# Kernel tuning notes

Measured on AMD Instinct MI355X. Metric: run time of the kernel, lower is better.

The kernel has to match this reference:

```python
import jax, jax.numpy as jnp
import numpy as np

DIM = 1024
NUM_EXPERTS = 8
N_TOKENS = 8192


def setup_inputs() -> dict:
    key = jax.random.key(0)
    ks = jax.random.split(key, 6)
    z_real = jax.random.normal(ks[0], (N_TOKENS, DIM), dtype=jnp.float32)
    z_imag = jax.random.normal(ks[1], (N_TOKENS, DIM), dtype=jnp.float32)
    # gate: nn.Linear(2*dim, E) -> weight [E, 2*dim], bias [E]
    Wg = jax.random.normal(ks[2], (NUM_EXPERTS, 2 * DIM), dtype=jnp.float32) * (1.0 / np.sqrt(2 * DIM))
    bg = jnp.zeros((NUM_EXPERTS,), dtype=jnp.float32)
    # experts: per-expert real/imag square weights [E, dim, dim] (nn.Linear layout: [out, in])
    Wr = jax.random.normal(ks[3], (NUM_EXPERTS, DIM, DIM), dtype=jnp.float32) * (1.0 / np.sqrt(DIM))
    Wi = jax.random.normal(ks[4], (NUM_EXPERTS, DIM, DIM), dtype=jnp.float32) * (1.0 / np.sqrt(DIM))
    return {"z_real": z_real, "z_imag": z_imag, "Wg": Wg, "bg": bg, "Wr": Wr, "Wi": Wi}


def reference(z_real, z_imag, Wg, bg, Wr, Wi):
    # gate over concat(real, imag)
    z_flat = jnp.concatenate([z_real, z_imag], axis=-1)            # [N, 2D]
    gates = jax.nn.softmax(z_flat @ Wg.T + bg, axis=-1)            # [N, E]
    # all-expert complex linear: y = x @ W^T with W [E, out, in]
    rr = jnp.einsum('ni,eoi->neo', z_real, Wr)                     # real @ Wr
    ii = jnp.einsum('ni,eoi->neo', z_imag, Wi)                     # imag @ Wi
    ri = jnp.einsum('ni,eoi->neo', z_imag, Wr)                     # imag @ Wr
    ir = jnp.einsum('ni,eoi->neo', z_real, Wi)                     # real @ Wi
    out_r = jnp.einsum('ne,neo->no', gates, rr - ii)               # [N, D]
    out_i = jnp.einsum('ne,neo->no', gates, ri + ir)               # [N, D]
    return jnp.stack([out_r, out_i], axis=0)                       # [2, N, D]
```

## Files before the change

kernel.cpp:

```cpp
#include <hip/hip_runtime.h>
#include <hip/hip_bf16.h>

#define NTOK 8192
#define DIM 1024
#define NEXP 8
#define NT 256
#define BK 64

typedef float f32x4 __attribute__((ext_vector_type(4)));
typedef short s16x8 __attribute__((ext_vector_type(8)));
typedef unsigned short u16;
typedef unsigned short u16x4 __attribute__((ext_vector_type(4)));

__device__ __forceinline__ u16 f2bf(float f) {
    __hip_bfloat16 h = __float2bfloat16(f);
    return *reinterpret_cast<u16*>(&h);
}
__device__ __forceinline__ float bf2f(u16 u) {
    unsigned v = ((unsigned)u) << 16;
    return __uint_as_float(v);
}

#define GLOAD16(gsrc, ldst)                                                     \
    __builtin_amdgcn_global_load_lds(                                           \
        (const __attribute__((address_space(1))) void*)(gsrc),                  \
        (__attribute__((address_space(3))) void*)(ldst), 16, 0, 0)

#define MFMA16(a, b, c) __builtin_amdgcn_mfma_f32_16x16x32_bf16((a), (b), (c), 0, 0, 0)
#define SGB() __builtin_amdgcn_sched_barrier(0)

__global__ __launch_bounds__(256) void gates_kernel(
    const float* __restrict__ zr, const float* __restrict__ zi,
    const float* __restrict__ Wg, const float* __restrict__ bg,
    float* __restrict__ gates)
{
    const int wave = threadIdx.x >> 6, lane = threadIdx.x & 63;
    const int n = blockIdx.x * 4 + wave;

    float v[32];
    const float* zrp = zr + (size_t)n * DIM;
    const float* zip = zi + (size_t)n * DIM;
#pragma unroll
    for (int j = 0; j < 16; ++j) v[j] = zrp[j * 64 + lane];
#pragma unroll
    for (int j = 0; j < 16; ++j) v[16 + j] = zip[j * 64 + lane];

    float s[NEXP];
#pragma unroll
    for (int e = 0; e < NEXP; ++e) {
        const float* wrow = Wg + (size_t)e * (2 * DIM);
        float a = 0.f;
#pragma unroll
        for (int j = 0; j < 32; ++j) a += v[j] * wrow[j * 64 + lane];
#pragma unroll
        for (int m = 32; m; m >>= 1) a += __shfl_xor(a, m);
        s[e] = a + bg[e];
    }
    float mx = s[0];
#pragma unroll
    for (int e = 1; e < NEXP; ++e) mx = fmaxf(mx, s[e]);
    float p[NEXP], sum = 0.f;
#pragma unroll
    for (int e = 0; e < NEXP; ++e) { p[e] = expf(s[e] - mx); sum += p[e]; }
    const float inv = 1.f / sum;
    if (lane == 0) {
#pragma unroll
        for (int e = 0; e < NEXP; ++e) gates[(size_t)n * NEXP + e] = p[e] * inv;
    }
}

__global__ __launch_bounds__(256) void cvt4_kernel(
    const float* __restrict__ zr, const float* __restrict__ zi,
    const float* __restrict__ Wr, const float* __restrict__ Wi,
    u16* __restrict__ zr16, u16* __restrict__ zi16,
    u16* __restrict__ Wr16, u16* __restrict__ Wi16)
{
    const size_t total = (size_t)NEXP * DIM * DIM / 4;
    for (size_t i = (size_t)blockIdx.x * 256 + threadIdx.x; i < total;
         i += (size_t)gridDim.x * 256) {
        f32x4 a = ((const f32x4*)zr)[i];
        f32x4 b = ((const f32x4*)zi)[i];
        f32x4 c = ((const f32x4*)Wr)[i];
        f32x4 d = ((const f32x4*)Wi)[i];
        u16x4 pa, pb, pc, pd;
#pragma unroll
        for (int j = 0; j < 4; ++j) {
            pa[j] = f2bf(a[j]); pb[j] = f2bf(b[j]);
            pc[j] = f2bf(c[j]); pd[j] = f2bf(d[j]);
        }
        ((u16x4*)zr16)[i] = pa;
        ((u16x4*)zi16)[i] = pb;
        ((u16x4*)Wr16)[i] = pc;
        ((u16x4*)Wi16)[i] = pd;
    }
}

__global__ __launch_bounds__(512, 2) void moe_gemm8(
    const u16* __restrict__ zr16, const u16* __restrict__ zi16,
    const u16* __restrict__ Wr16, const u16* __restrict__ Wi16,
    const float* __restrict__ gates, float* __restrict__ out)
{
    extern __shared__ u16 lds[];

    const int linear = blockIdx.x + 32 * (blockIdx.y + 4 * blockIdx.z);
    const int xcd = linear & 7;
    const int bm = xcd * 4 + ((linear >> 3) & 3);
    const int grp2 = linear >> 5;
    const int bn = grp2 & 3;
    const int sel = grp2 >> 2;

    const int tid = threadIdx.x;
    const int lane = tid & 63;
    const int wid = tid >> 6;
    const int wr = wid >> 2;
    const int wc = wid & 3;

    const int srow = tid >> 3;
    const int schunk = (tid & 7) ^ (srow & 7);
    int arow[4], gidx[4], brow[4];
#pragma unroll
    for (int j = 0; j < 4; ++j) {
        const int gr = bm * 256 + srow + j * 64;
        arow[j] = gr * DIM + schunk * 8;
        gidx[j] = gr * NEXP;
        brow[j] = (bn * 256 + srow + j * 64) * DIM + schunk * 8;
    }

    const int cg = lane >> 4;
    const int l7 = lane & 7;
    const int ach0 = (cg ^ l7) * 8;
    const int ach1 = ((4 + cg) ^ l7) * 8;
    const int arbase = (wr * 128 + (lane & 15)) * BK;
    const int brbase = (wc * 64 + (lane & 15)) * BK;

    f32x4 acc[8][4];
#pragma unroll
    for (int m = 0; m < 8; ++m)
#pragma unroll
        for (int n = 0; n < 4; ++n) acc[m][n] = (f32x4){0.f, 0.f, 0.f, 0.f};

    const u16* Asrc = sel ? zi16 : zr16;
    const u16* Bseg = Wr16;
    float sg[4];
#pragma unroll
    for (int j = 0; j < 4; ++j) sg[j] = gates[gidx[j]];

    {
        s16x8 ga[4];
#pragma unroll
        for (int j = 0; j < 4; ++j) ga[j] = *(const s16x8*)(Asrc + arow[j]);
#pragma unroll
        for (int i = 0; i < 4; ++i)
            GLOAD16(Bseg + brow[i], &lds[32768 + (i * 512 + tid) * 8]);
#pragma unroll
        for (int i = 0; i < 4; ++i)
            GLOAD16(Bseg + brow[i] + 64, &lds[32768 + 16384 + (i * 512 + tid) * 8]);
#pragma unroll
        for (int j = 0; j < 4; ++j) {
            s16x8 w;
#pragma unroll
            for (int q = 0; q < 8; ++q)
                w[q] = (short)f2bf(bf2f((u16)ga[j][q]) * sg[j]);
            *(s16x8*)&lds[(tid + j * 512) * 8] = w;
        }
        asm volatile("s_waitcnt vmcnt(4) lgkmcnt(0)" ::: "memory");
        __builtin_amdgcn_s_barrier();
    }

    int br = 0;
#pragma unroll 1
    for (int t = 0; t < NT; ++t) {
        const int tn1 = t + 1, tn2 = t + 2;
        if ((tn1 & 15) == 0) {
            const int seg = tn1 >> 4;
            const int e = (seg >> 1) & 7;
            const int half = seg & 1;
            Asrc = (half ^ sel) ? zi16 : zr16;
            const float sgn = (sel == 0 && half == 1) ? -1.f : 1.f;
#pragma unroll
            for (int j = 0; j < 4; ++j) sg[j] = sgn * gates[gidx[j] + e];
        }
        if ((tn2 & 15) == 0) {
            const int seg = tn2 >> 4;
            const int e = (seg >> 1) & 7;
            Bseg = ((seg & 1) ? Wi16 : Wr16) + (size_t)e * DIM * DIM;
        }
        const int ka = (tn1 & 15) << 6;
        const int kb = (tn2 & 15) << 6;
        const int bs = (br + 2) % 3;
        const int ab = ((t & 1) << 14) + arbase;
        const int bb = 32768 + br * 16384 + brbase;
        const int sa = ((tn1 & 1) << 14);
        const int sbB = 32768 + bs * 16384;

        s16x8 ga[4];
#pragma unroll
        for (int j = 0; j < 4; ++j) ga[j] = *(const s16x8*)(Asrc + arow[j] + ka);
        GLOAD16(Bseg + brow[0] + kb, &lds[sbB + (0 * 512 + tid) * 8]);
        GLOAD16(Bseg + brow[1] + kb, &lds[sbB + (1 * 512 + tid) * 8]);
        GLOAD16(Bseg + brow[2] + kb, &lds[sbB + (2 * 512 + tid) * 8]);
        GLOAD16(Bseg + brow[3] + kb, &lds[sbB + (3 * 512 + tid) * 8]);

        s16x8 b0[4], a0[4], a1[4], b1[4], a2[4], a3[4];
#pragma unroll
        for (int n = 0; n < 4; ++n) b0[n] = *(const s16x8*)&lds[bb + n * 1024 + ach0];
#pragma unroll
        for (int m = 0; m < 4; ++m) a0[m] = *(const s16x8*)&lds[ab + m * 1024 + ach0];
#pragma unroll
        for (int m = 0; m < 4; ++m) a1[m] = *(const s16x8*)&lds[ab + (m + 4) * 1024 + ach0];
        SGB();
        __builtin_amdgcn_s_setprio(1);
#pragma unroll
        for (int m = 0; m < 4; ++m)
#pragma unroll
            for (int n = 0; n < 4; ++n) acc[m][n] = MFMA16(a0[m], b0[n], acc[m][n]);
        __builtin_amdgcn_s_setprio(0);

#pragma unroll
        for (int n = 0; n < 4; ++n) b1[n] = *(const s16x8*)&lds[bb + n * 1024 + ach1];
#pragma unroll
        for (int m = 0; m < 4; ++m) a2[m] = *(const s16x8*)&lds[ab + m * 1024 + ach1];
        SGB();
        __builtin_amdgcn_s_setprio(1);
#pragma unroll
        for (int m = 0; m < 4; ++m)
#pragma unroll
            for (int n = 0; n < 4; ++n) acc[m + 4][n] = MFMA16(a1[m], b0[n], acc[m + 4][n]);
        __builtin_amdgcn_s_setprio(0);

#pragma unroll
        for (int j = 0; j < 2; ++j) {
            s16x8 w;
#pragma unroll
            for (int q = 0; q < 8; ++q)
                w[q] = (short)f2bf(bf2f((u16)ga[j][q]) * sg[j]);
            *(s16x8*)&lds[sa + (tid + j * 512) * 8] = w;
        }
#pragma unroll
        for (int m = 0; m < 4; ++m) a3[m] = *(const s16x8*)&lds[ab + (m + 4) * 1024 + ach1];
        SGB();
        __builtin_amdgcn_s_setprio(1);
#pragma unroll
        for (int m = 0; m < 4; ++m)
#pragma unroll
            for (int n = 0; n < 4; ++n) acc[m][n] = MFMA16(a2[m], b1[n], acc[m][n]);
        __builtin_amdgcn_s_setprio(0);

#pragma unroll
        for (int j = 2; j < 4; ++j) {
            s16x8 w;
#pragma unroll
            for (int q = 0; q < 8; ++q)
                w[q] = (short)f2bf(bf2f((u16)ga[j][q]) * sg[j]);
            *(s16x8*)&lds[sa + (tid + j * 512) * 8] = w;
        }
        __builtin_amdgcn_s_setprio(1);
#pragma unroll
        for (int m = 0; m < 4; ++m)
#pragma unroll
            for (int n = 0; n < 4; ++n) acc[m + 4][n] = MFMA16(a3[m], b1[n], acc[m + 4][n]);
        __builtin_amdgcn_s_setprio(0);

        asm volatile("s_waitcnt vmcnt(4) lgkmcnt(0)" ::: "memory");
        __builtin_amdgcn_s_barrier();

        br = (br == 2) ? 0 : br + 1;
    }
    asm volatile("s_waitcnt vmcnt(0)" ::: "memory");

    float* op = out + (size_t)sel * NTOK * DIM;
    const int col0 = bn * 256 + wc * 64 + (lane & 15);
    const int row0 = bm * 256 + wr * 128 + ((lane >> 4) << 2);
#pragma unroll
    for (int m = 0; m < 8; ++m)
#pragma unroll
        for (int n = 0; n < 4; ++n)
#pragma unroll
            for (int j = 0; j < 4; ++j)
                op[(size_t)(row0 + m * 16 + j) * DIM + col0 + n * 16] = acc[m][n][j];
}

extern "C" void kernel_launch(void* const* d_in, const int* in_sizes, int n_in,
                              void* d_out, int out_size, void* d_ws, size_t ws_size,
                              hipStream_t stream) {
    const float* zr = (const float*)d_in[0];
    const float* zi = (const float*)d_in[1];
    const float* Wg = (const float*)d_in[2];
    const float* bg = (const float*)d_in[3];
    const float* Wr = (const float*)d_in[4];
    const float* Wi = (const float*)d_in[5];
    float* out = (float*)d_out;

    const size_t NELEM = (size_t)NEXP * DIM * DIM;
    u16* zr16 = (u16*)d_ws;
    u16* zi16 = zr16 + NELEM;
    u16* Wr16 = zi16 + NELEM;
    u16* Wi16 = Wr16 + NELEM;
    float* gates = (float*)(Wi16 + NELEM);

    cvt4_kernel<<<2048, 256, 0, stream>>>(zr, zi, Wr, Wi, zr16, zi16, Wr16, Wi16);
    gates_kernel<<<NTOK / 4, 256, 0, stream>>>(zr, zi, Wg, bg, gates);

    hipFuncSetAttribute((const void*)moe_gemm8,
                        hipFuncAttributeMaxDynamicSharedMemorySize, 163840);
    dim3 grid(NTOK / 256, DIM / 256, 2);
    moe_gemm8<<<grid, 512, 163840, stream>>>(zr16, zi16, Wr16, Wi16, gates, out);
}
```

Before: 542.6 us.

## Restructure GEMM pipeline: triple-buffer A, double-buffer B, prefetch first A fragments

Changes the shared-memory buffering in the MoE GEMM main loop. The scaled activation tile A is now triple-buffered and written two steps ahead, and the weight tile B is double-buffered and loaded one step ahead. The first A register fragments for the next iteration are loaded before the loop-end barrier, and the barrier waits on all global loads while leaving some LDS reads outstanding. The goal is to hide LDS read latency across the barrier and to spread the activation scaling work between MFMA groups. The trade-offs are a shorter global-load lookahead for B and extra registers held for the prefetched fragments.

```diff
diff --git a/kernel.cpp b/kernel.cpp
--- a/kernel.cpp
+++ b/kernel.cpp
@@ -95,7 +95,7 @@
     }
 }
 
-__global__ __launch_bounds__(512, 2) void moe_gemm8(
+__global__ __launch_bounds__(512, 2) void moe_gemm12(
     const u16* __restrict__ zr16, const u16* __restrict__ zi16,
     const u16* __restrict__ Wr16, const u16* __restrict__ Wi16,
     const float* __restrict__ gates, float* __restrict__ out)
@@ -146,33 +146,43 @@
     for (int j = 0; j < 4; ++j) sg[j] = gates[gidx[j]];
 
     {
-        s16x8 ga[4];
-#pragma unroll
-        for (int j = 0; j < 4; ++j) ga[j] = *(const s16x8*)(Asrc + arow[j]);
-#pragma unroll
-        for (int i = 0; i < 4; ++i)
-            GLOAD16(Bseg + brow[i], &lds[32768 + (i * 512 + tid) * 8]);
-#pragma unroll
-        for (int i = 0; i < 4; ++i)
-            GLOAD16(Bseg + brow[i] + 64, &lds[32768 + 16384 + (i * 512 + tid) * 8]);
+        s16x8 ga0[4], ga1[4];
 #pragma unroll
         for (int j = 0; j < 4; ++j) {
-            s16x8 w;
-#pragma unroll
-            for (int q = 0; q < 8; ++q)
-                w[q] = (short)f2bf(bf2f((u16)ga[j][q]) * sg[j]);
-            *(s16x8*)&lds[(tid + j * 512) * 8] = w;
-        }
-        asm volatile("s_waitcnt vmcnt(4) lgkmcnt(0)" ::: "memory");
+            ga0[j] = *(const s16x8*)(Asrc + arow[j]);
+            ga1[j] = *(const s16x8*)(Asrc + arow[j] + BK);
+        }
+#pragma unroll
+        for (int q = 0; q < 4; ++q)
+            GLOAD16(Bseg + brow[q], &lds[49152 + (q * 512 + tid) * 8]);
+#pragma unroll
+        for (int j = 0; j < 4; ++j) {
+            s16x8 w0, w1;
+#pragma unroll
+            for (int e = 0; e < 8; ++e) {
+                w0[e] = (short)f2bf(bf2f((u16)ga0[j][e]) * sg[j]);
+                w1[e] = (short)f2bf(bf2f((u16)ga1[j][e]) * sg[j]);
+            }
+            *(s16x8*)&lds[(tid + j * 512) * 8] = w0;
+            *(s16x8*)&lds[16384 + (tid + j * 512) * 8] = w1;
+        }
+        asm volatile("s_waitcnt vmcnt(0) lgkmcnt(0)" ::: "memory");
         __builtin_amdgcn_s_barrier();
     }
 
-    int br = 0;
+    s16x8 a0p[4];
+#pragma unroll
+    for (int m = 0; m < 4; ++m)
+        a0p[m] = *(const s16x8*)&lds[arbase + m * 1024 + ach0];
+
+    int ars = 0;
+    int aws = 2;
+    int brs = 0;
 #pragma unroll 1
     for (int t = 0; t < NT; ++t) {
-        const int tn1 = t + 1, tn2 = t + 2;
-        if ((tn1 & 15) == 0) {
-            const int seg = tn1 >> 4;
+        const int t1 = t + 1, t2 = t + 2;
+        if ((t2 & 15) == 0) {
+            const int seg = t2 >> 4;
             const int e = (seg >> 1) & 7;
             const int half = seg & 1;
             Asrc = (half ^ sel) ? zi16 : zr16;
@@ -180,19 +190,21 @@
 #pragma unroll
             for (int j = 0; j < 4; ++j) sg[j] = sgn * gates[gidx[j] + e];
         }
-        if ((tn2 & 15) == 0) {
-            const int seg = tn2 >> 4;
+        if ((t1 & 15) == 0) {
+            const int seg = t1 >> 4;
             const int e = (seg >> 1) & 7;
             Bseg = ((seg & 1) ? Wi16 : Wr16) + (size_t)e * DIM * DIM;
         }
-        const int ka = (tn1 & 15) << 6;
-        const int kb = (tn2 & 15) << 6;
-        const int bs = (br + 2) % 3;
-        const int ab = ((t & 1) << 14) + arbase;
-        const int bb = 32768 + br * 16384 + brbase;
-        const int sa = ((tn1 & 1) << 14);
-        const int sbB = 32768 + bs * 16384;
-
+        const int ka = (t2 & 15) << 6;
+        const int kb = (t1 & 15) << 6;
+        const int ab = ars * 16384 + arbase;
+        const int bb = 49152 + brs * 16384 + brbase;
+        const int sa = aws * 16384;
+        const int sbB = 49152 + (brs ^ 1) * 16384;
+
+        s16x8 b0[4];
+#pragma unroll
+        for (int n = 0; n < 4; ++n) b0[n] = *(const s16x8*)&lds[bb + n * 1024 + ach0];
         s16x8 ga[4];
 #pragma unroll
         for (int j = 0; j < 4; ++j) ga[j] = *(const s16x8*)(Asrc + arow[j] + ka);
@@ -200,12 +212,7 @@
         GLOAD16(Bseg + brow[1] + kb, &lds[sbB + (1 * 512 + tid) * 8]);
         GLOAD16(Bseg + brow[2] + kb, &lds[sbB + (2 * 512 + tid) * 8]);
         GLOAD16(Bseg + brow[3] + kb, &lds[sbB + (3 * 512 + tid) * 8]);
-
-        s16x8 b0[4], a0[4], a1[4], b1[4], a2[4], a3[4];
-#pragma unroll
-        for (int n = 0; n < 4; ++n) b0[n] = *(const s16x8*)&lds[bb + n * 1024 + ach0];
-#pragma unroll
-        for (int m = 0; m < 4; ++m) a0[m] = *(const s16x8*)&lds[ab + m * 1024 + ach0];
+        s16x8 a1[4];
 #pragma unroll
         for (int m = 0; m < 4; ++m) a1[m] = *(const s16x8*)&lds[ab + (m + 4) * 1024 + ach0];
         SGB();
@@ -213,9 +220,18 @@
 #pragma unroll
         for (int m = 0; m < 4; ++m)
 #pragma unroll
-            for (int n = 0; n < 4; ++n) acc[m][n] = MFMA16(a0[m], b0[n], acc[m][n]);
+            for (int n = 0; n < 4; ++n) acc[m][n] = MFMA16(a0p[m], b0[n], acc[m][n]);
         __builtin_amdgcn_s_setprio(0);
 
+#pragma unroll
+        for (int j = 0; j < 2; ++j) {
+            s16x8 w;
+#pragma unroll
+            for (int e = 0; e < 8; ++e)
+                w[e] = (short)f2bf(bf2f((u16)ga[j][e]) * sg[j]);
+            *(s16x8*)&lds[sa + (tid + j * 512) * 8] = w;
+        }
+        s16x8 b1[4], a2[4];
 #pragma unroll
         for (int n = 0; n < 4; ++n) b1[n] = *(const s16x8*)&lds[bb + n * 1024 + ach1];
 #pragma unroll
@@ -229,13 +245,14 @@
         __builtin_amdgcn_s_setprio(0);
 
 #pragma unroll
-        for (int j = 0; j < 2; ++j) {
+        for (int j = 2; j < 4; ++j) {
             s16x8 w;
 #pragma unroll
-            for (int q = 0; q < 8; ++q)
-                w[q] = (short)f2bf(bf2f((u16)ga[j][q]) * sg[j]);
+            for (int e = 0; e < 8; ++e)
+                w[e] = (short)f2bf(bf2f((u16)ga[j][e]) * sg[j]);
             *(s16x8*)&lds[sa + (tid + j * 512) * 8] = w;
         }
+        s16x8 a3[4];
 #pragma unroll
         for (int m = 0; m < 4; ++m) a3[m] = *(const s16x8*)&lds[ab + (m + 4) * 1024 + ach1];
         SGB();
@@ -246,14 +263,11 @@
             for (int n = 0; n < 4; ++n) acc[m][n] = MFMA16(a2[m], b1[n], acc[m][n]);
         __builtin_amdgcn_s_setprio(0);
 
-#pragma unroll
-        for (int j = 2; j < 4; ++j) {
-            s16x8 w;
-#pragma unroll
-            for (int q = 0; q < 8; ++q)
-                w[q] = (short)f2bf(bf2f((u16)ga[j][q]) * sg[j]);
-            *(s16x8*)&lds[sa + (tid + j * 512) * 8] = w;
-        }
+        const int arn = (ars == 2) ? 0 : ars + 1;
+        const int abn = arn * 16384 + arbase;
+#pragma unroll
+        for (int m = 0; m < 4; ++m) a0p[m] = *(const s16x8*)&lds[abn + m * 1024 + ach0];
+        SGB();
         __builtin_amdgcn_s_setprio(1);
 #pragma unroll
         for (int m = 0; m < 4; ++m)
@@ -261,12 +275,14 @@
             for (int n = 0; n < 4; ++n) acc[m + 4][n] = MFMA16(a3[m], b1[n], acc[m + 4][n]);
         __builtin_amdgcn_s_setprio(0);
 
-        asm volatile("s_waitcnt vmcnt(4) lgkmcnt(0)" ::: "memory");
+        asm volatile("s_waitcnt vmcnt(0) lgkmcnt(4)" ::: "memory");
         __builtin_amdgcn_s_barrier();
 
-        br = (br == 2) ? 0 : br + 1;
-    }
-    asm volatile("s_waitcnt vmcnt(0)" ::: "memory");
+        ars = arn;
+        aws = (aws == 2) ? 0 : aws + 1;
+        brs ^= 1;
+    }
+    asm volatile("s_waitcnt vmcnt(0) lgkmcnt(0)" ::: "memory");
 
     float* op = out + (size_t)sel * NTOK * DIM;
     const int col0 = bn * 256 + wc * 64 + (lane & 15);
@@ -301,8 +317,8 @@
     cvt4_kernel<<<2048, 256, 0, stream>>>(zr, zi, Wr, Wi, zr16, zi16, Wr16, Wi16);
     gates_kernel<<<NTOK / 4, 256, 0, stream>>>(zr, zi, Wg, bg, gates);
 
-    hipFuncSetAttribute((const void*)moe_gemm8,
+    hipFuncSetAttribute((const void*)moe_gemm12,
                         hipFuncAttributeMaxDynamicSharedMemorySize, 163840);
     dim3 grid(NTOK / 256, DIM / 256, 2);
-    moe_gemm8<<<grid, 512, 163840, stream>>>(zr16, zi16, Wr16, Wi16, gates, out);
-}
+    moe_gemm12<<<grid, 512, 163840, stream>>>(zr16, zi16, Wr16, Wi16, gates, out);
+}
```

New measurement: 550.8 us. No clear change (+1.5%).

## Replace triple-buffered B pipeline with double-buffered ping-pong and extra barriers

Applied to the files above, without the earlier changes.

The B-operand prefetch moves from a three-deep ring (two tiles ahead) to a two-buffer ping-pong (one tile ahead), which cuts LDS use from 160 KB to 128 KB. The main loop is regrouped into two 8x4 MFMA phases, each with a partial lgkmcnt wait and a mid-phase workgroup barrier, in a ping-pong style schedule. The goal is tighter wave synchronisation and less LDS footprint. In exchange, global-load latency is hidden less deeply, a full vmcnt(0) wait now runs every iteration, and there are more barriers per tile.

```diff
diff --git a/kernel.cpp b/kernel.cpp
--- a/kernel.cpp
+++ b/kernel.cpp
@@ -95,7 +95,7 @@
     }
 }
 
-__global__ __launch_bounds__(512, 2) void moe_gemm8(
+__global__ __launch_bounds__(512, 2) void moe_gemm13(
     const u16* __restrict__ zr16, const u16* __restrict__ zi16,
     const u16* __restrict__ Wr16, const u16* __restrict__ Wi16,
     const float* __restrict__ gates, float* __restrict__ out)
@@ -146,127 +146,101 @@
     for (int j = 0; j < 4; ++j) sg[j] = gates[gidx[j]];
 
     {
-        s16x8 ga[4];
-#pragma unroll
-        for (int j = 0; j < 4; ++j) ga[j] = *(const s16x8*)(Asrc + arow[j]);
-#pragma unroll
-        for (int i = 0; i < 4; ++i)
-            GLOAD16(Bseg + brow[i], &lds[32768 + (i * 512 + tid) * 8]);
-#pragma unroll
-        for (int i = 0; i < 4; ++i)
-            GLOAD16(Bseg + brow[i] + 64, &lds[32768 + 16384 + (i * 512 + tid) * 8]);
+        s16x8 ga0[4];
+#pragma unroll
+        for (int j = 0; j < 4; ++j) ga0[j] = *(const s16x8*)(Asrc + arow[j]);
+#pragma unroll
+        for (int q = 0; q < 4; ++q)
+            GLOAD16(Bseg + brow[q], &lds[32768 + (q * 512 + tid) * 8]);
 #pragma unroll
         for (int j = 0; j < 4; ++j) {
             s16x8 w;
 #pragma unroll
-            for (int q = 0; q < 8; ++q)
-                w[q] = (short)f2bf(bf2f((u16)ga[j][q]) * sg[j]);
+            for (int e = 0; e < 8; ++e)
+                w[e] = (short)f2bf(bf2f((u16)ga0[j][e]) * sg[j]);
             *(s16x8*)&lds[(tid + j * 512) * 8] = w;
         }
-        asm volatile("s_waitcnt vmcnt(4) lgkmcnt(0)" ::: "memory");
-        __builtin_amdgcn_s_barrier();
-    }
-
-    int br = 0;
+        asm volatile("s_waitcnt vmcnt(0) lgkmcnt(0)" ::: "memory");
+        __builtin_amdgcn_s_barrier();
+    }
+
+    int buf = 0;
 #pragma unroll 1
     for (int t = 0; t < NT; ++t) {
-        const int tn1 = t + 1, tn2 = t + 2;
-        if ((tn1 & 15) == 0) {
-            const int seg = tn1 >> 4;
+        const int t1 = t + 1;
+        if ((t1 & 15) == 0) {
+            const int seg = t1 >> 4;
             const int e = (seg >> 1) & 7;
             const int half = seg & 1;
             Asrc = (half ^ sel) ? zi16 : zr16;
+            Bseg = (half ? Wi16 : Wr16) + (size_t)e * DIM * DIM;
             const float sgn = (sel == 0 && half == 1) ? -1.f : 1.f;
 #pragma unroll
             for (int j = 0; j < 4; ++j) sg[j] = sgn * gates[gidx[j] + e];
         }
-        if ((tn2 & 15) == 0) {
-            const int seg = tn2 >> 4;
-            const int e = (seg >> 1) & 7;
-            Bseg = ((seg & 1) ? Wi16 : Wr16) + (size_t)e * DIM * DIM;
-        }
-        const int ka = (tn1 & 15) << 6;
-        const int kb = (tn2 & 15) << 6;
-        const int bs = (br + 2) % 3;
-        const int ab = ((t & 1) << 14) + arbase;
-        const int bb = 32768 + br * 16384 + brbase;
-        const int sa = ((tn1 & 1) << 14);
-        const int sbB = 32768 + bs * 16384;
+        const int ka = (t1 & 15) << 6;
+        const int ab = buf * 16384 + arbase;
+        const int bb = 32768 + buf * 16384 + brbase;
+        const int sa = (buf ^ 1) * 16384;
+        const int sb = 32768 + (buf ^ 1) * 16384;
 
         s16x8 ga[4];
 #pragma unroll
         for (int j = 0; j < 4; ++j) ga[j] = *(const s16x8*)(Asrc + arow[j] + ka);
-        GLOAD16(Bseg + brow[0] + kb, &lds[sbB + (0 * 512 + tid) * 8]);
-        GLOAD16(Bseg + brow[1] + kb, &lds[sbB + (1 * 512 + tid) * 8]);
-        GLOAD16(Bseg + brow[2] + kb, &lds[sbB + (2 * 512 + tid) * 8]);
-        GLOAD16(Bseg + brow[3] + kb, &lds[sbB + (3 * 512 + tid) * 8]);
-
-        s16x8 b0[4], a0[4], a1[4], b1[4], a2[4], a3[4];
+        GLOAD16(Bseg + brow[0] + ka, &lds[sb + (0 * 512 + tid) * 8]);
+        GLOAD16(Bseg + brow[1] + ka, &lds[sb + (1 * 512 + tid) * 8]);
+        GLOAD16(Bseg + brow[2] + ka, &lds[sb + (2 * 512 + tid) * 8]);
+        GLOAD16(Bseg + brow[3] + ka, &lds[sb + (3 * 512 + tid) * 8]);
+
+        s16x8 b0[4], a01[8];
 #pragma unroll
         for (int n = 0; n < 4; ++n) b0[n] = *(const s16x8*)&lds[bb + n * 1024 + ach0];
 #pragma unroll
-        for (int m = 0; m < 4; ++m) a0[m] = *(const s16x8*)&lds[ab + m * 1024 + ach0];
-#pragma unroll
-        for (int m = 0; m < 4; ++m) a1[m] = *(const s16x8*)&lds[ab + (m + 4) * 1024 + ach0];
+        for (int m = 0; m < 8; ++m) a01[m] = *(const s16x8*)&lds[ab + m * 1024 + ach0];
+        asm volatile("s_waitcnt lgkmcnt(8)" ::: "memory");
+        SGB();
+        __builtin_amdgcn_s_barrier();
+        asm volatile("s_waitcnt lgkmcnt(0)" ::: "memory");
         SGB();
         __builtin_amdgcn_s_setprio(1);
 #pragma unroll
-        for (int m = 0; m < 4; ++m)
-#pragma unroll
-            for (int n = 0; n < 4; ++n) acc[m][n] = MFMA16(a0[m], b0[n], acc[m][n]);
+        for (int m = 0; m < 8; ++m)
+#pragma unroll
+            for (int n = 0; n < 4; ++n) acc[m][n] = MFMA16(a01[m], b0[n], acc[m][n]);
         __builtin_amdgcn_s_setprio(0);
-
+        SGB();
+        __builtin_amdgcn_s_barrier();
+
+        s16x8 b1[4], a23[8];
 #pragma unroll
         for (int n = 0; n < 4; ++n) b1[n] = *(const s16x8*)&lds[bb + n * 1024 + ach1];
 #pragma unroll
-        for (int m = 0; m < 4; ++m) a2[m] = *(const s16x8*)&lds[ab + m * 1024 + ach1];
+        for (int m = 0; m < 8; ++m) a23[m] = *(const s16x8*)&lds[ab + m * 1024 + ach1];
+#pragma unroll
+        for (int j = 0; j < 4; ++j) {
+            s16x8 w;
+#pragma unroll
+            for (int e = 0; e < 8; ++e)
+                w[e] = (short)f2bf(bf2f((u16)ga[j][e]) * sg[j]);
+            *(s16x8*)&lds[sa + (tid + j * 512) * 8] = w;
+        }
+        asm volatile("s_waitcnt lgkmcnt(8)" ::: "memory");
+        SGB();
+        __builtin_amdgcn_s_barrier();
+        asm volatile("s_waitcnt lgkmcnt(0)" ::: "memory");
         SGB();
         __builtin_amdgcn_s_setprio(1);
 #pragma unroll
-        for (int m = 0; m < 4; ++m)
-#pragma unroll
-            for (int n = 0; n < 4; ++n) acc[m + 4][n] = MFMA16(a1[m], b0[n], acc[m + 4][n]);
+        for (int m = 0; m < 8; ++m)
+#pragma unroll
+            for (int n = 0; n < 4; ++n) acc[m][n] = MFMA16(a23[m], b1[n], acc[m][n]);
         __builtin_amdgcn_s_setprio(0);
-
-#pragma unroll
-        for (int j = 0; j < 2; ++j) {
-            s16x8 w;
-#pragma unroll
-            for (int q = 0; q < 8; ++q)
-                w[q] = (short)f2bf(bf2f((u16)ga[j][q]) * sg[j]);
-            *(s16x8*)&lds[sa + (tid + j * 512) * 8] = w;
-        }
-#pragma unroll
-        for (int m = 0; m < 4; ++m) a3[m] = *(const s16x8*)&lds[ab + (m + 4) * 1024 + ach1];
-        SGB();
-        __builtin_amdgcn_s_setprio(1);
-#pragma unroll
-        for (int m = 0; m < 4; ++m)
-#pragma unroll
-            for (int n = 0; n < 4; ++n) acc[m][n] = MFMA16(a2[m], b1[n], acc[m][n]);
-        __builtin_amdgcn_s_setprio(0);
-
-#pragma unroll
-        for (int j = 2; j < 4; ++j) {
-            s16x8 w;
-#pragma unroll
-            for (int q = 0; q < 8; ++q)
-                w[q] = (short)f2bf(bf2f((u16)ga[j][q]) * sg[j]);
-            *(s16x8*)&lds[sa + (tid + j * 512) * 8] = w;
-        }
-        __builtin_amdgcn_s_setprio(1);
-#pragma unroll
-        for (int m = 0; m < 4; ++m)
-#pragma unroll
-            for (int n = 0; n < 4; ++n) acc[m + 4][n] = MFMA16(a3[m], b1[n], acc[m + 4][n]);
-        __builtin_amdgcn_s_setprio(0);
-
-        asm volatile("s_waitcnt vmcnt(4) lgkmcnt(0)" ::: "memory");
-        __builtin_amdgcn_s_barrier();
-
-        br = (br == 2) ? 0 : br + 1;
-    }
-    asm volatile("s_waitcnt vmcnt(0)" ::: "memory");
+        asm volatile("s_waitcnt vmcnt(0)" ::: "memory");
+        SGB();
+        __builtin_amdgcn_s_barrier();
+
+        buf ^= 1;
+    }
 
     float* op = out + (size_t)sel * NTOK * DIM;
     const int col0 = bn * 256 + wc * 64 + (lane & 15);
@@ -301,8 +275,8 @@
     cvt4_kernel<<<2048, 256, 0, stream>>>(zr, zi, Wr, Wi, zr16, zi16, Wr16, Wi16);
     gates_kernel<<<NTOK / 4, 256, 0, stream>>>(zr, zi, Wg, bg, gates);
 
-    hipFuncSetAttribute((const void*)moe_gemm8,
-                        hipFuncAttributeMaxDynamicSharedMemorySize, 163840);
+    hipFuncSetAttribute((const void*)moe_gemm13,
+                        hipFuncAttributeMaxDynamicSharedMemorySize, 131072);
     dim3 grid(NTOK / 256, DIM / 256, 2);
-    moe_gemm8<<<grid, 512, 163840, stream>>>(zr16, zi16, Wr16, Wi16, gates, out);
-}
+    moe_gemm13<<<grid, 512, 131072, stream>>>(zr16, zi16, Wr16, Wi16, gates, out);
+}
```

Measured after the change: 574.3 us. +5.8%, slower.

## Precompute gate-scaled bf16 activations per expert and stream both operands via LDS DMA

Applied to the files above, without the earlier changes.

Gates are now computed first, and a new prez kernel writes 16 gate-scaled bf16 copies of the activations (one per expert for real and imag), plus a negated Wi copy so the subtraction folds into the weights. The new GEMM loads A directly into LDS with global_load_lds (triple-buffered) instead of loading into registers, scaling, and storing, and uses finer-grained barriers between MFMA phases. This removes per-tile VALU scaling and register staging from the GEMM main loop. In exchange it writes and reads far more workspace (16x the activation volume, about 256MB in bf16) and adds a barrier-heavy schedule, and it falls back to the old path when the workspace is too small.

```diff
diff --git a/kernel.cpp b/kernel.cpp
--- a/kernel.cpp
+++ b/kernel.cpp
@@ -6,6 +6,7 @@
 #define NEXP 8
 #define NT 256
 #define BK 64
+#define NELEMZ ((size_t)NTOK * DIM)
 
 typedef float f32x4 __attribute__((ext_vector_type(4)));
 typedef short s16x8 __attribute__((ext_vector_type(8)));
@@ -69,13 +70,237 @@
     }
 }
 
+__global__ __launch_bounds__(256) void prez_kernel(
+    const float* __restrict__ zr, const float* __restrict__ zi,
+    const float* __restrict__ gates, u16* __restrict__ zvar)
+{
+    const size_t total = NELEMZ / 4;
+    for (size_t i = (size_t)blockIdx.x * 256 + threadIdx.x; i < total;
+         i += (size_t)gridDim.x * 256) {
+        const int n = (int)(i >> 8);
+        f32x4 a = ((const f32x4*)zr)[i];
+        f32x4 b = ((const f32x4*)zi)[i];
+        float g[NEXP];
+#pragma unroll
+        for (int e = 0; e < NEXP; ++e) g[e] = gates[(size_t)n * NEXP + e];
+#pragma unroll
+        for (int e = 0; e < NEXP; ++e) {
+            u16x4 pa, pb;
+#pragma unroll
+            for (int j = 0; j < 4; ++j) {
+                pa[j] = f2bf(a[j] * g[e]);
+                pb[j] = f2bf(b[j] * g[e]);
+            }
+            ((u16x4*)(zvar + (size_t)e * NELEMZ))[i] = pa;
+            ((u16x4*)(zvar + (size_t)(8 + e) * NELEMZ))[i] = pb;
+        }
+    }
+}
+
+__global__ __launch_bounds__(256) void wcvt3_kernel(
+    const float* __restrict__ Wr, const float* __restrict__ Wi,
+    u16* __restrict__ Wr16, u16* __restrict__ Wi16, u16* __restrict__ WiN16)
+{
+    const size_t total = NELEMZ / 4;
+    for (size_t i = (size_t)blockIdx.x * 256 + threadIdx.x; i < total;
+         i += (size_t)gridDim.x * 256) {
+        f32x4 c = ((const f32x4*)Wr)[i];
+        f32x4 d = ((const f32x4*)Wi)[i];
+        u16x4 pc, pd, pn;
+#pragma unroll
+        for (int j = 0; j < 4; ++j) {
+            pc[j] = f2bf(c[j]);
+            pd[j] = f2bf(d[j]);
+            pn[j] = f2bf(-d[j]);
+        }
+        ((u16x4*)Wr16)[i] = pc;
+        ((u16x4*)Wi16)[i] = pd;
+        ((u16x4*)WiN16)[i] = pn;
+    }
+}
+
+__global__ __launch_bounds__(512, 2) void moe_gemm14(
+    const u16* __restrict__ zvar,
+    const u16* __restrict__ Wr16, const u16* __restrict__ Wi16,
+    const u16* __restrict__ WiN16, float* __restrict__ out)
+{
+    extern __shared__ u16 lds[];
+
+    const int linear = blockIdx.x + 32 * (blockIdx.y + 4 * blockIdx.z);
+    const int xcd = linear & 7;
+    const int bm = xcd * 4 + ((linear >> 3) & 3);
+    const int grp2 = linear >> 5;
+    const int bn = grp2 & 3;
+    const int sel = grp2 >> 2;
+
+    const int tid = threadIdx.x;
+    const int lane = tid & 63;
+    const int wid = tid >> 6;
+    const int wr = wid >> 2;
+    const int wc = wid & 3;
+
+    const int srow = tid >> 3;
+    const int schunk = (tid & 7) ^ (srow & 7);
+    int arow[4], brow[4];
+#pragma unroll
+    for (int j = 0; j < 4; ++j) {
+        arow[j] = (bm * 256 + srow + j * 64) * DIM + schunk * 8;
+        brow[j] = (bn * 256 + srow + j * 64) * DIM + schunk * 8;
+    }
+
+    const int cg = lane >> 4;
+    const int l7 = lane & 7;
+    const int ach0 = (cg ^ l7) * 8;
+    const int ach1 = ((4 + cg) ^ l7) * 8;
+    const int arbase = (wr * 128 + (lane & 15)) * BK;
+    const int brbase = (wc * 64 + (lane & 15)) * BK;
+
+    f32x4 acc[8][4];
+#pragma unroll
+    for (int m = 0; m < 8; ++m)
+#pragma unroll
+        for (int n = 0; n < 4; ++n) acc[m][n] = (f32x4){0.f, 0.f, 0.f, 0.f};
+
+    const u16* Avar = zvar + (size_t)(sel ? 8 : 0) * NELEMZ;
+    const u16* Bh0 = Wr16;
+    const u16* Bh1 = sel ? Wi16 : WiN16;
+    const u16* Bseg = Bh0;
+
+    {
+#pragma unroll
+        for (int j = 0; j < 4; ++j) GLOAD16(Avar + arow[j], &lds[(j * 512 + tid) * 8]);
+#pragma unroll
+        for (int j = 0; j < 4; ++j) GLOAD16(Avar + arow[j] + BK, &lds[16384 + (j * 512 + tid) * 8]);
+#pragma unroll
+        for (int j = 0; j < 4; ++j) GLOAD16(Bseg + brow[j], &lds[49152 + (j * 512 + tid) * 8]);
+        asm volatile("s_waitcnt vmcnt(0)" ::: "memory");
+        __builtin_amdgcn_s_barrier();
+    }
+
+    int ars = 0;
+#pragma unroll 1
+    for (int t = 0; t < NT; ++t) {
+        const int t1 = t + 1, t2 = t + 2;
+        if ((t1 & 15) == 0) {
+            const int seg = t1 >> 4;
+            const int e = (seg >> 1) & 7;
+            Bseg = ((seg & 1) ? Bh1 : Bh0) + (size_t)e * DIM * DIM;
+        }
+        if ((t2 & 15) == 0) {
+            const int seg = t2 >> 4;
+            const int e = (seg >> 1) & 7;
+            const int half = seg & 1;
+            Avar = zvar + (size_t)(((half ^ sel) ? 8 : 0) + e) * NELEMZ;
+        }
+        const int kb1 = (t1 & 15) << 6;
+        const int ka2 = (t2 & 15) << 6;
+        const int aw = (ars == 0) ? 2 : ars - 1;
+        const int brs = t & 1;
+        const int ab = ars * 16384 + arbase;
+        const int bb = 49152 + brs * 16384 + brbase;
+        const int sa = aw * 16384;
+        const int sb = 49152 + (brs ^ 1) * 16384;
+
+        GLOAD16(Bseg + brow[0] + kb1, &lds[sb + (0 * 512 + tid) * 8]);
+        GLOAD16(Bseg + brow[1] + kb1, &lds[sb + (1 * 512 + tid) * 8]);
+        GLOAD16(Bseg + brow[2] + kb1, &lds[sb + (2 * 512 + tid) * 8]);
+        GLOAD16(Bseg + brow[3] + kb1, &lds[sb + (3 * 512 + tid) * 8]);
+        s16x8 b0[4], a0[4];
+#pragma unroll
+        for (int n = 0; n < 4; ++n) b0[n] = *(const s16x8*)&lds[bb + n * 1024 + ach0];
+#pragma unroll
+        for (int m = 0; m < 4; ++m) a0[m] = *(const s16x8*)&lds[ab + m * 1024 + ach0];
+        SGB();
+        __builtin_amdgcn_s_barrier();
+        asm volatile("s_waitcnt lgkmcnt(0)" ::: "memory");
+        SGB();
+        __builtin_amdgcn_s_setprio(1);
+#pragma unroll
+        for (int m = 0; m < 4; ++m)
+#pragma unroll
+            for (int n = 0; n < 4; ++n) acc[m][n] = MFMA16(a0[m], b0[n], acc[m][n]);
+        __builtin_amdgcn_s_setprio(0);
+        SGB();
+        __builtin_amdgcn_s_barrier();
+
+        GLOAD16(Avar + arow[0] + ka2, &lds[sa + (0 * 512 + tid) * 8]);
+        GLOAD16(Avar + arow[1] + ka2, &lds[sa + (1 * 512 + tid) * 8]);
+        GLOAD16(Avar + arow[2] + ka2, &lds[sa + (2 * 512 + tid) * 8]);
+        GLOAD16(Avar + arow[3] + ka2, &lds[sa + (3 * 512 + tid) * 8]);
+        s16x8 a1[4];
+#pragma unroll
+        for (int m = 0; m < 4; ++m) a1[m] = *(const s16x8*)&lds[ab + (m + 4) * 1024 + ach0];
+        SGB();
+        __builtin_amdgcn_s_barrier();
+        asm volatile("s_waitcnt lgkmcnt(0)" ::: "memory");
+        SGB();
+        __builtin_amdgcn_s_setprio(1);
+#pragma unroll
+        for (int m = 0; m < 4; ++m)
+#pragma unroll
+            for (int n = 0; n < 4; ++n) acc[m + 4][n] = MFMA16(a1[m], b0[n], acc[m + 4][n]);
+        __builtin_amdgcn_s_setprio(0);
+        SGB();
+        __builtin_amdgcn_s_barrier();
+
+        s16x8 b1[4], a2[4];
+#pragma unroll
+        for (int n = 0; n < 4; ++n) b1[n] = *(const s16x8*)&lds[bb + n * 1024 + ach1];
+#pragma unroll
+        for (int m = 0; m < 4; ++m) a2[m] = *(const s16x8*)&lds[ab + m * 1024 + ach1];
+        SGB();
+        __builtin_amdgcn_s_barrier();
+        asm volatile("s_waitcnt lgkmcnt(0)" ::: "memory");
+        SGB();
+        __builtin_amdgcn_s_setprio(1);
+#pragma unroll
+        for (int m = 0; m < 4; ++m)
+#pragma unroll
+            for (int n = 0; n < 4; ++n) acc[m][n] = MFMA16(a2[m], b1[n], acc[m][n]);
+        __builtin_amdgcn_s_setprio(0);
+        SGB();
+        __builtin_amdgcn_s_barrier();
+
+        s16x8 a3[4];
+#pragma unroll
+        for (int m = 0; m < 4; ++m) a3[m] = *(const s16x8*)&lds[ab + (m + 4) * 1024 + ach1];
+        SGB();
+        __builtin_amdgcn_s_barrier();
+        asm volatile("s_waitcnt lgkmcnt(0)" ::: "memory");
+        SGB();
+        __builtin_amdgcn_s_setprio(1);
+#pragma unroll
+        for (int m = 0; m < 4; ++m)
+#pragma unroll
+            for (int n = 0; n < 4; ++n) acc[m + 4][n] = MFMA16(a3[m], b1[n], acc[m + 4][n]);
+        __builtin_amdgcn_s_setprio(0);
+        asm volatile("s_waitcnt vmcnt(4)" ::: "memory");
+        SGB();
+        __builtin_amdgcn_s_barrier();
+
+        ars = (ars == 2) ? 0 : ars + 1;
+    }
+    asm volatile("s_waitcnt vmcnt(0)" ::: "memory");
+
+    float* op = out + (size_t)sel * NTOK * DIM;
+    const int col0 = bn * 256 + wc * 64 + (lane & 15);
+    const int row0 = bm * 256 + wr * 128 + ((lane >> 4) << 2);
+#pragma unroll
+    for (int m = 0; m < 8; ++m)
+#pragma unroll
+        for (int n = 0; n < 4; ++n)
+#pragma unroll
+            for (int j = 0; j < 4; ++j)
+                op[(size_t)(row0 + m * 16 + j) * DIM + col0 + n * 16] = acc[m][n][j];
+}
+
 __global__ __launch_bounds__(256) void cvt4_kernel(
     const float* __restrict__ zr, const float* __restrict__ zi,
     const float* __restrict__ Wr, const float* __restrict__ Wi,
     u16* __restrict__ zr16, u16* __restrict__ zi16,
     u16* __restrict__ Wr16, u16* __restrict__ Wi16)
 {
-    const size_t total = (size_t)NEXP * DIM * DIM / 4;
+    const size_t total = NELEMZ / 4;
     for (size_t i = (size_t)blockIdx.x * 256 + threadIdx.x; i < total;
          i += (size_t)gridDim.x * 256) {
         f32x4 a = ((const f32x4*)zr)[i];
@@ -101,20 +326,16 @@
     const float* __restrict__ gates, float* __restrict__ out)
 {
     extern __shared__ u16 lds[];
-
     const int linear = blockIdx.x + 32 * (blockIdx.y + 4 * blockIdx.z);
     const int xcd = linear & 7;
     const int bm = xcd * 4 + ((linear >> 3) & 3);
     const int grp2 = linear >> 5;
     const int bn = grp2 & 3;
     const int sel = grp2 >> 2;
-
     const int tid = threadIdx.x;
     const int lane = tid & 63;
     const int wid = tid >> 6;
-    const int wr = wid >> 2;
-    const int wc = wid & 3;
-
+    const int wr = wid >> 2, wc = wid & 3;
     const int srow = tid >> 3;
     const int schunk = (tid & 7) ^ (srow & 7);
     int arow[4], gidx[4], brow[4];
@@ -125,48 +346,39 @@
         gidx[j] = gr * NEXP;
         brow[j] = (bn * 256 + srow + j * 64) * DIM + schunk * 8;
     }
-
-    const int cg = lane >> 4;
-    const int l7 = lane & 7;
+    const int cg = lane >> 4, l7 = lane & 7;
     const int ach0 = (cg ^ l7) * 8;
     const int ach1 = ((4 + cg) ^ l7) * 8;
     const int arbase = (wr * 128 + (lane & 15)) * BK;
     const int brbase = (wc * 64 + (lane & 15)) * BK;
-
     f32x4 acc[8][4];
 #pragma unroll
     for (int m = 0; m < 8; ++m)
 #pragma unroll
         for (int n = 0; n < 4; ++n) acc[m][n] = (f32x4){0.f, 0.f, 0.f, 0.f};
-
     const u16* Asrc = sel ? zi16 : zr16;
     const u16* Bseg = Wr16;
     float sg[4];
 #pragma unroll
     for (int j = 0; j < 4; ++j) sg[j] = gates[gidx[j]];
-
     {
         s16x8 ga[4];
 #pragma unroll
         for (int j = 0; j < 4; ++j) ga[j] = *(const s16x8*)(Asrc + arow[j]);
 #pragma unroll
-        for (int i = 0; i < 4; ++i)
-            GLOAD16(Bseg + brow[i], &lds[32768 + (i * 512 + tid) * 8]);
-#pragma unroll
-        for (int i = 0; i < 4; ++i)
-            GLOAD16(Bseg + brow[i] + 64, &lds[32768 + 16384 + (i * 512 + tid) * 8]);
+        for (int i = 0; i < 4; ++i) GLOAD16(Bseg + brow[i], &lds[32768 + (i * 512 + tid) * 8]);
+#pragma unroll
+        for (int i = 0; i < 4; ++i) GLOAD16(Bseg + brow[i] + 64, &lds[32768 + 16384 + (i * 512 + tid) * 8]);
 #pragma unroll
         for (int j = 0; j < 4; ++j) {
             s16x8 w;
 #pragma unroll
-            for (int q = 0; q < 8; ++q)
-                w[q] = (short)f2bf(bf2f((u16)ga[j][q]) * sg[j]);
+            for (int q = 0; q < 8; ++q) w[q] = (short)f2bf(bf2f((u16)ga[j][q]) * sg[j]);
             *(s16x8*)&lds[(tid + j * 512) * 8] = w;
         }
         asm volatile("s_waitcnt vmcnt(4) lgkmcnt(0)" ::: "memory");
         __builtin_amdgcn_s_barrier();
     }
-
     int br = 0;
 #pragma unroll 1
     for (int t = 0; t < NT; ++t) {
@@ -187,12 +399,11 @@
         }
         const int ka = (tn1 & 15) << 6;
         const int kb = (tn2 & 15) << 6;
-        const int bs = (br + 2) % 3;
+        const int bs = (br == 0) ? 2 : br - 1;
         const int ab = ((t & 1) << 14) + arbase;
         const int bb = 32768 + br * 16384 + brbase;
         const int sa = ((tn1 & 1) << 14);
         const int sbB = 32768 + bs * 16384;
-
         s16x8 ga[4];
 #pragma unroll
         for (int j = 0; j < 4; ++j) ga[j] = *(const s16x8*)(Asrc + arow[j] + ka);
@@ -200,7 +411,6 @@
         GLOAD16(Bseg + brow[1] + kb, &lds[sbB + (1 * 512 + tid) * 8]);
         GLOAD16(Bseg + brow[2] + kb, &lds[sbB + (2 * 512 + tid) * 8]);
         GLOAD16(Bseg + brow[3] + kb, &lds[sbB + (3 * 512 + tid) * 8]);
-
         s16x8 b0[4], a0[4], a1[4], b1[4], a2[4], a3[4];
 #pragma unroll
         for (int n = 0; n < 4; ++n) b0[n] = *(const s16x8*)&lds[bb + n * 1024 + ach0];
@@ -215,7 +425,6 @@
 #pragma unroll
             for (int n = 0; n < 4; ++n) acc[m][n] = MFMA16(a0[m], b0[n], acc[m][n]);
         __builtin_amdgcn_s_setprio(0);
-
 #pragma unroll
         for (int n = 0; n < 4; ++n) b1[n] = *(const s16x8*)&lds[bb + n * 1024 + ach1];
 #pragma unroll
@@ -227,13 +436,11 @@
 #pragma unroll
             for (int n = 0; n < 4; ++n) acc[m + 4][n] = MFMA16(a1[m], b0[n], acc[m + 4][n]);
         __builtin_amdgcn_s_setprio(0);
-
 #pragma unroll
         for (int j = 0; j < 2; ++j) {
             s16x8 w;
 #pragma unroll
-            for (int q = 0; q < 8; ++q)
-                w[q] = (short)f2bf(bf2f((u16)ga[j][q]) * sg[j]);
+            for (int q = 0; q < 8; ++q) w[q] = (short)f2bf(bf2f((u16)ga[j][q]) * sg[j]);
             *(s16x8*)&lds[sa + (tid + j * 512) * 8] = w;
         }
 #pragma unroll
@@ -245,13 +452,11 @@
 #pragma unroll
             for (int n = 0; n < 4; ++n) acc[m][n] = MFMA16(a2[m], b1[n], acc[m][n]);
         __builtin_amdgcn_s_setprio(0);
-
 #pragma unroll
         for (int j = 2; j < 4; ++j) {
             s16x8 w;
 #pragma unroll
-            for (int q = 0; q < 8; ++q)
-                w[q] = (short)f2bf(bf2f((u16)ga[j][q]) * sg[j]);
+            for (int q = 0; q < 8; ++q) w[q] = (short)f2bf(bf2f((u16)ga[j][q]) * sg[j]);
             *(s16x8*)&lds[sa + (tid + j * 512) * 8] = w;
         }
         __builtin_amdgcn_s_setprio(1);
@@ -260,14 +465,11 @@
 #pragma unroll
             for (int n = 0; n < 4; ++n) acc[m + 4][n] = MFMA16(a3[m], b1[n], acc[m + 4][n]);
         __builtin_amdgcn_s_setprio(0);
-
         asm volatile("s_waitcnt vmcnt(4) lgkmcnt(0)" ::: "memory");
         __builtin_amdgcn_s_barrier();
-
         br = (br == 2) ? 0 : br + 1;
     }
     asm volatile("s_waitcnt vmcnt(0)" ::: "memory");
-
     float* op = out + (size_t)sel * NTOK * DIM;
     const int col0 = bn * 256 + wc * 64 + (lane & 15);
     const int row0 = bm * 256 + wr * 128 + ((lane >> 4) << 2);
@@ -291,18 +493,37 @@
     const float* Wi = (const float*)d_in[5];
     float* out = (float*)d_out;
 
-    const size_t NELEM = (size_t)NEXP * DIM * DIM;
-    u16* zr16 = (u16*)d_ws;
-    u16* zi16 = zr16 + NELEM;
-    u16* Wr16 = zi16 + NELEM;
-    u16* Wi16 = Wr16 + NELEM;
-    float* gates = (float*)(Wi16 + NELEM);
-
-    cvt4_kernel<<<2048, 256, 0, stream>>>(zr, zi, Wr, Wi, zr16, zi16, Wr16, Wi16);
-    gates_kernel<<<NTOK / 4, 256, 0, stream>>>(zr, zi, Wg, bg, gates);
-
-    hipFuncSetAttribute((const void*)moe_gemm8,
-                        hipFuncAttributeMaxDynamicSharedMemorySize, 163840);
-    dim3 grid(NTOK / 256, DIM / 256, 2);
-    moe_gemm8<<<grid, 512, 163840, stream>>>(zr16, zi16, Wr16, Wi16, gates, out);
-}
+    const size_t need_new = (16 + 3) * NELEMZ * sizeof(u16)
+                          + (size_t)NTOK * NEXP * sizeof(float) + 1024;
+
+    if (ws_size >= need_new) {
+        u16* zvar = (u16*)d_ws;
+        u16* Wr16 = zvar + 16 * NELEMZ;
+        u16* Wi16 = Wr16 + NELEMZ;
+        u16* WiN16 = Wi16 + NELEMZ;
+        float* gates = (float*)(WiN16 + NELEMZ);
+
+        gates_kernel<<<NTOK / 4, 256, 0, stream>>>(zr, zi, Wg, bg, gates);
+        prez_kernel<<<2048, 256, 0, stream>>>(zr, zi, gates, zvar);
+        wcvt3_kernel<<<2048, 256, 0, stream>>>(Wr, Wi, Wr16, Wi16, WiN16);
+
+        hipFuncSetAttribute((const void*)moe_gemm14,
+                            hipFuncAttributeMaxDynamicSharedMemorySize, 163840);
+        dim3 grid(NTOK / 256, DIM / 256, 2);
+        moe_gemm14<<<grid, 512, 163840, stream>>>(zvar, Wr16, Wi16, WiN16, out);
+    } else {
+        u16* zr16 = (u16*)d_ws;
+        u16* zi16 = zr16 + NELEMZ;
+        u16* Wr16 = zi16 + NELEMZ;
+        u16* Wi16 = Wr16 + NELEMZ;
+        float* gates = (float*)(Wi16 + NELEMZ);
+
+        cvt4_kernel<<<2048, 256, 0, stream>>>(zr, zi, Wr, Wi, zr16, zi16, Wr16, Wi16);
+        gates_kernel<<<NTOK / 4, 256, 0, stream>>>(zr, zi, Wg, bg, gates);
+
+        hipFuncSetAttribute((const void*)moe_gemm8,
+                            hipFuncAttributeMaxDynamicSharedMemorySize, 163840);
+        dim3 grid(NTOK / 256, DIM / 256, 2);
+        moe_gemm8<<<grid, 512, 163840, stream>>>(zr16, zi16, Wr16, Wi16, gates, out);
+    }
+}
```

Result: no change. 537.6 us (-0.9%).
